# Kernel optimization log

Measured on AMD Instinct MI355X. Metric: run time of the kernel, lower is better.

## Reference

```python
import jax, jax.numpy as jnp
import numpy as np

N, E, IN, H, OUT = 50000, 800000, 256, 128, 64


def setup_inputs() -> dict:
    key = jax.random.key(0)
    ks = jax.random.split(key, 4)
    x = jax.random.normal(ks[0], (N, IN), dtype=jnp.float32)
    edge_index = jax.random.randint(ks[1], (2, E), 0, N, dtype=jnp.int64)
    W1 = jax.random.normal(ks[2], (IN, H), dtype=jnp.float32) / np.float32(np.sqrt(IN))
    b1 = jnp.zeros((H,), jnp.float32)
    W2 = jax.random.normal(ks[3], (H, OUT), dtype=jnp.float32) / np.float32(np.sqrt(H))
    b2 = jnp.zeros((OUT,), jnp.float32)
    return {"x": x, "edge_index": edge_index, "W1": W1, "b1": b1, "W2": W2, "b2": b2}


def _gcn_conv(x, W, b, src, dst, norm, n):
    # PyG GCNConv: linear transform, then symmetric-normalized aggregation, then bias
    h = x @ W                                        # [n, d_out]
    agg = jax.ops.segment_sum(h[src] * norm[:, None], dst, num_segments=n)
    return agg + b


def reference(x, edge_index, W1, b1, W2, b2):
    n = x.shape[0]
    loop = jnp.arange(n, dtype=edge_index.dtype)
    # add self-loops (GCNConv default add_self_loops=True)
    src = jnp.concatenate([edge_index[0], loop])
    dst = jnp.concatenate([edge_index[1], loop])
    # symmetric normalization deg^{-1/2} A_hat deg^{-1/2}
    deg = jax.ops.segment_sum(jnp.ones(src.shape, jnp.float32), dst, num_segments=n)
    dinv = jnp.where(deg > 0, jax.lax.rsqrt(deg), 0.0)
    norm = dinv[src] * dinv[dst]                     # [E + n]
    h = jax.nn.relu(_gcn_conv(x, W1, b1, src, dst, norm, n))
    return _gcn_conv(h, W2, b2, src, dst, norm, n)
```

## Files before the change

### kernel.cpp

```cpp
#include <hip/hip_runtime.h>


#define DI 256
#define DH 128
#define DO 64
#define NBC 98
#define EPB 8192
#define P4CAP 12288

typedef unsigned short ushort;
typedef unsigned int uint;
using bf16x8 = __attribute__((ext_vector_type(8))) short;
using f32x4  = __attribute__((ext_vector_type(4))) float;

__device__ __forceinline__ ushort f2b(float f) {
    union { float f; uint u; } v; v.f = f;
    uint r = (v.u + 0x7fffu + ((v.u >> 16) & 1u)) >> 16;
    return (ushort)r;
}
__device__ __forceinline__ float blo(uint v) { return __uint_as_float(v << 16); }
__device__ __forceinline__ float bhi(uint v) { return __uint_as_float(v & 0xffff0000u); }

__global__ __launch_bounds__(256) void hist_k(const int* __restrict__ dst,
                                              int* __restrict__ hist, int E,
                                              const float* __restrict__ W1,
                                              ushort* __restrict__ W1t,
                                              const float* __restrict__ W2,
                                              ushort* __restrict__ W2t) {
    __shared__ int lh[NBC];
    const int blk = blockIdx.x;
    for (int i = threadIdx.x; i < NBC; i += 256) lh[i] = 0;
    __syncthreads();
    const int gid = blk * 256 + threadIdx.x;
#pragma unroll
    for (int r = 0; r < 2; ++r) {
        int idx = gid + r * 25088;
        if (idx < DI * DH) {
            int m = idx / DI, k = idx % DI;
            W1t[idx] = f2b(W1[(long)k * DH + m]);
        }
    }
    if (gid < DH * DO) {
        int m = gid / DH, k = gid % DH;
        W2t[gid] = f2b(W2[(long)k * DO + m]);
    }
    const int base = blk * EPB, end = min(base + EPB, E);
    for (int e = base + threadIdx.x; e < end; e += 256)
        atomicAdd(&lh[dst[e] >> 9], 1);
    __syncthreads();
    for (int i = threadIdx.x; i < NBC; i += 256) hist[blk * NBC + i] = lh[i];
}

__global__ void scan_mat(int* __restrict__ hist, int* __restrict__ boff,
                         int* __restrict__ off, int nbp, int n, int E) {
    __shared__ int mat[NBC * NBC];
    __shared__ int tot[NBC], bo[NBC];
    const int tid = threadIdx.x;
    const int tote = nbp * NBC;
    for (int i = tid; i < tote; i += 256) mat[i] = hist[i];
    __syncthreads();
    if (tid < NBC) {
        int run = 0;
        for (int b = 0; b < nbp; ++b) {
            int v = mat[b * NBC + tid];
            mat[b * NBC + tid] = run;
            run += v;
        }
        tot[tid] = run;
    }
    __syncthreads();
    if (tid == 0) {
        int r = 0;
        for (int c = 0; c < NBC; ++c) { bo[c] = r; r += tot[c]; }
        boff[NBC] = r;
        off[n] = E;
    }
    __syncthreads();
    if (tid < NBC) boff[tid] = bo[tid];
    for (int i = tid; i < tote; i += 256) hist[i] = mat[i] + bo[i % NBC];
}

__global__ __launch_bounds__(256) void part_k(const int* __restrict__ src,
                                              const int* __restrict__ dst,
                                              const int* __restrict__ hist,
                                              uint* __restrict__ pairs, int E) {
    __shared__ int cur[NBC];
    const int blk = blockIdx.x;
    for (int i = threadIdx.x; i < NBC; i += 256) cur[i] = hist[blk * NBC + i];
    __syncthreads();
    const int base = blk * EPB, end = min(base + EPB, E);
    for (int e = base + threadIdx.x; e < end; e += 256) {
        int d = dst[e], s = src[e];
        int slot = atomicAdd(&cur[d >> 9], 1);
        pairs[slot] = ((uint)s << 9) | (uint)(d & 511);
    }
}

__global__ __launch_bounds__(256) void bucket_k(const uint* __restrict__ pairs,
                                                const int* __restrict__ boff,
                                                int* __restrict__ off,
                                                float* __restrict__ dinv,
                                                int* __restrict__ csr, int n) {
    __shared__ int lh[512], lcur[512], tsum[256];
    __shared__ int sorted[P4CAP];
    const int tid = threadIdx.x;
    const int cb = blockIdx.x;
    const int b0 = boff[cb], b1 = boff[cb + 1];
    const int cnt = b1 - b0;
    lh[tid] = 0; lh[tid + 256] = 0;
    __syncthreads();
    for (int i = tid; i < cnt; i += 256) atomicAdd(&lh[pairs[b0 + i] & 511], 1);
    __syncthreads();
    const int s0 = lh[2 * tid], s1 = lh[2 * tid + 1];
    const int s = s0 + s1;
    tsum[tid] = s;
    __syncthreads();
    for (int o = 1; o < 256; o <<= 1) {
        int t = (tid >= o) ? tsum[tid - o] : 0;
        __syncthreads();
        tsum[tid] += t;
        __syncthreads();
    }
    const int ex = tsum[tid] - s;
    lcur[2 * tid] = ex; lcur[2 * tid + 1] = ex + s0;
    {
        int node = cb * 512 + 2 * tid;
        if (node < n)     { off[node]     = b0 + ex;      dinv[node]     = rsqrtf((float)s0 + 1.f); }
        if (node + 1 < n) { off[node + 1] = b0 + ex + s0; dinv[node + 1] = rsqrtf((float)s1 + 1.f); }
    }
    __syncthreads();
    for (int i = tid; i < cnt; i += 256) {
        uint v = pairs[b0 + i];
        int slot = atomicAdd(&lcur[v & 511], 1);
        if (slot < P4CAP) sorted[slot] = (int)(v >> 9);
    }
    __syncthreads();
    const int cs = min(cnt, P4CAP);
    for (int i = tid; i < cs; i += 256) csr[b0 + i] = sorted[i];
}

template<int K, int M, bool INF32>
__global__ __launch_bounds__(256) void mfma_gemm(const void* __restrict__ Xv,
                                                 const ushort* __restrict__ Wt,
                                                 const float* __restrict__ dinv,
                                                 ushort* __restrict__ Y, int n) {
    constexpr int ROWB = K * 2;
    constexpr int CT = M / 64;
    __shared__ ushort Xs[64 * K];
    const int t = threadIdx.x;
    const int r0 = blockIdx.x * 64;

    {
        const int row = t >> 2, q = t & 3;
        const int gr = r0 + row;
        if (INF32) {
            const float* Xr = (const float*)Xv + (long)gr * K;
#pragma unroll
            for (int j = 0; j < K / 32; ++j) {
                float4 a = make_float4(0.f, 0.f, 0.f, 0.f), b = a;
                if (gr < n) {
                    a = *(const float4*)&Xr[q * 8 + j * 32];
                    b = *(const float4*)&Xr[q * 8 + j * 32 + 4];
                }
                ushort u[8] = {f2b(a.x), f2b(a.y), f2b(a.z), f2b(a.w),
                               f2b(b.x), f2b(b.y), f2b(b.z), f2b(b.w)};
                int byte = row * ROWB + q * 16 + j * 64;
                byte ^= (row & 7) << 4;
                *(uint4*)((char*)Xs + byte) = *(const uint4*)u;
            }
        } else {
            const ushort* Xr = (const ushort*)Xv + (long)gr * K;
#pragma unroll
            for (int j = 0; j < K / 32; ++j) {
                uint4 v = make_uint4(0u, 0u, 0u, 0u);
                if (gr < n) v = *(const uint4*)&Xr[q * 8 + j * 32];
                int byte = row * ROWB + q * 16 + j * 64;
                byte ^= (row & 7) << 4;
                *(uint4*)((char*)Xs + byte) = v;
            }
        }
    }
    __syncthreads();

    const int w  = t >> 6;
    const int l  = t & 63;
    const int lr = l & 15;
    const int lg = l >> 4;
    f32x4 acc[4][CT] = {};

#pragma unroll
    for (int ks = 0; ks < K / 32; ++ks) {
        bf16x8 bfr[CT];
#pragma unroll
        for (int ct = 0; ct < CT; ++ct) {
            int col = w * (M / 4) + ct * 16 + lr;
            bfr[ct] = *(const bf16x8*)&Wt[(long)col * K + ks * 32 + lg * 8];
        }
        bf16x8 afr[4];
#pragma unroll
        for (int rt = 0; rt < 4; ++rt) {
            int row = rt * 16 + lr;
            int byte = row * ROWB + ks * 64 + lg * 16;
            byte ^= (row & 7) << 4;
            afr[rt] = *(const bf16x8*)((const char*)Xs + byte);
        }
#pragma unroll
        for (int rt = 0; rt < 4; ++rt)
#pragma unroll
            for (int ct = 0; ct < CT; ++ct)
                acc[rt][ct] = __builtin_amdgcn_mfma_f32_16x16x32_bf16(
                    afr[rt], bfr[ct], acc[rt][ct], 0, 0, 0);
    }

#pragma unroll
    for (int rt = 0; rt < 4; ++rt)
#pragma unroll
        for (int i = 0; i < 4; ++i) {
            int gr2 = r0 + rt * 16 + lg * 4 + i;
            if (gr2 < n) {
                float dv = dinv[gr2];
#pragma unroll
                for (int ct = 0; ct < CT; ++ct) {
                    int col = w * (M / 4) + ct * 16 + lr;
                    Y[(long)gr2 * M + col] = f2b(dv * acc[rt][ct][i]);
                }
            }
        }
}

__global__ __launch_bounds__(256) void gather_half(const int* __restrict__ off,
                                                   const int* __restrict__ csr,
                                                   const ushort* __restrict__ Hs,
                                                   const float* __restrict__ dinv,
                                                   const float* __restrict__ b1,
                                                   ushort* __restrict__ h, int n) {
    const int wv = threadIdx.x >> 6, ln = threadIdx.x & 63;
    const int grp = ln >> 3, j = ln & 7;
    const int half = blockIdx.x & 1;
    const int i = (blockIdx.x >> 1) * 4 + wv;
    if (i >= n) return;
    const uint4* H4 = (const uint4*)Hs;
    const int cb = half * 8 + j;
    float a0[8] = {}, a1[8] = {};
    const int k0 = off[i], ke = off[i + 1];
    int k = k0 + grp;
    for (; k + 8 < ke; k += 16) {
        uint4 va = H4[(long)csr[k] * 16 + cb];
        uint4 vb = H4[(long)csr[k + 8] * 16 + cb];
        a0[0] += blo(va.x); a0[1] += bhi(va.x);
        a0[2] += blo(va.y); a0[3] += bhi(va.y);
        a0[4] += blo(va.z); a0[5] += bhi(va.z);
        a0[6] += blo(va.w); a0[7] += bhi(va.w);
        a1[0] += blo(vb.x); a1[1] += bhi(vb.x);
        a1[2] += blo(vb.y); a1[3] += bhi(vb.y);
        a1[4] += blo(vb.z); a1[5] += bhi(vb.z);
        a1[6] += blo(vb.w); a1[7] += bhi(vb.w);
    }
    if (k < ke) {
        uint4 va = H4[(long)csr[k] * 16 + cb];
        a0[0] += blo(va.x); a0[1] += bhi(va.x);
        a0[2] += blo(va.y); a0[3] += bhi(va.y);
        a0[4] += blo(va.z); a0[5] += bhi(va.z);
        a0[6] += blo(va.w); a0[7] += bhi(va.w);
    }
    if (grp == 0) {
        uint4 va = H4[(long)i * 16 + cb];
        a1[0] += blo(va.x); a1[1] += bhi(va.x);
        a1[2] += blo(va.y); a1[3] += bhi(va.y);
        a1[4] += blo(va.z); a1[5] += bhi(va.z);
        a1[6] += blo(va.w); a1[7] += bhi(va.w);
    }
    float acc[8];
#pragma unroll
    for (int m = 0; m < 8; ++m) {
        acc[m] = a0[m] + a1[m];
        acc[m] += __shfl_xor(acc[m], 8, 64);
        acc[m] += __shfl_xor(acc[m], 16, 64);
        acc[m] += __shfl_xor(acc[m], 32, 64);
    }
    if (grp == 0) {
        float di = dinv[i];
        float4 bb0 = ((const float4*)b1)[cb * 2];
        float4 bb1 = ((const float4*)b1)[cb * 2 + 1];
        ushort u[8];
        u[0] = f2b(fmaxf(di * acc[0] + bb0.x, 0.f));
        u[1] = f2b(fmaxf(di * acc[1] + bb0.y, 0.f));
        u[2] = f2b(fmaxf(di * acc[2] + bb0.z, 0.f));
        u[3] = f2b(fmaxf(di * acc[3] + bb0.w, 0.f));
        u[4] = f2b(fmaxf(di * acc[4] + bb1.x, 0.f));
        u[5] = f2b(fmaxf(di * acc[5] + bb1.y, 0.f));
        u[6] = f2b(fmaxf(di * acc[6] + bb1.z, 0.f));
        u[7] = f2b(fmaxf(di * acc[7] + bb1.w, 0.f));
        *(uint4*)&h[(long)i * DH + cb * 8] = *(const uint4*)u;
    }
}

__global__ __launch_bounds__(256) void gather_out(const int* __restrict__ off,
                                                  const int* __restrict__ csr,
                                                  const ushort* __restrict__ Hs,
                                                  const float* __restrict__ dinv,
                                                  const float* __restrict__ b,
                                                  float* __restrict__ Y, int n) {
    const int wv = threadIdx.x >> 6, ln = threadIdx.x & 63;
    const int grp = ln >> 3, j = ln & 7;
    const int i = blockIdx.x * 4 + wv;
    if (i >= n) return;
    const uint4* H4 = (const uint4*)Hs;
    float a0[8] = {}, a1[8] = {}, a2[8] = {}, a3[8] = {};
    const int k0 = off[i], ke = off[i + 1];
    int k = k0 + grp;
    for (; k + 24 < ke; k += 32) {
        uint4 va = H4[(long)csr[k]      * 8 + j];
        uint4 vb = H4[(long)csr[k + 8]  * 8 + j];
        uint4 vc = H4[(long)csr[k + 16] * 8 + j];
        uint4 vd = H4[(long)csr[k + 24] * 8 + j];
        a0[0] += blo(va.x); a0[1] += bhi(va.x); a0[2] += blo(va.y); a0[3] += bhi(va.y);
        a0[4] += blo(va.z); a0[5] += bhi(va.z); a0[6] += blo(va.w); a0[7] += bhi(va.w);
        a1[0] += blo(vb.x); a1[1] += bhi(vb.x); a1[2] += blo(vb.y); a1[3] += bhi(vb.y);
        a1[4] += blo(vb.z); a1[5] += bhi(vb.z); a1[6] += blo(vb.w); a1[7] += bhi(vb.w);
        a2[0] += blo(vc.x); a2[1] += bhi(vc.x); a2[2] += blo(vc.y); a2[3] += bhi(vc.y);
        a2[4] += blo(vc.z); a2[5] += bhi(vc.z); a2[6] += blo(vc.w); a2[7] += bhi(vc.w);
        a3[0] += blo(vd.x); a3[1] += bhi(vd.x); a3[2] += blo(vd.y); a3[3] += bhi(vd.y);
        a3[4] += blo(vd.z); a3[5] += bhi(vd.z); a3[6] += blo(vd.w); a3[7] += bhi(vd.w);
    }
    for (; k < ke; k += 8) {
        uint4 va = H4[(long)csr[k] * 8 + j];
        a0[0] += blo(va.x); a0[1] += bhi(va.x); a0[2] += blo(va.y); a0[3] += bhi(va.y);
        a0[4] += blo(va.z); a0[5] += bhi(va.z); a0[6] += blo(va.w); a0[7] += bhi(va.w);
    }
    if (grp == 0) {
        uint4 va = H4[(long)i * 8 + j];
        a1[0] += blo(va.x); a1[1] += bhi(va.x); a1[2] += blo(va.y); a1[3] += bhi(va.y);
        a1[4] += blo(va.z); a1[5] += bhi(va.z); a1[6] += blo(va.w); a1[7] += bhi(va.w);
    }
    float acc[8];
#pragma unroll
    for (int m = 0; m < 8; ++m) {
        acc[m] = (a0[m] + a1[m]) + (a2[m] + a3[m]);
        acc[m] += __shfl_xor(acc[m], 8, 64);
        acc[m] += __shfl_xor(acc[m], 16, 64);
        acc[m] += __shfl_xor(acc[m], 32, 64);
    }
    if (grp == 0) {
        float di = dinv[i];
        float4 b0 = ((const float4*)b)[j * 2];
        float4 b1 = ((const float4*)b)[j * 2 + 1];
        float4 o0, o1;
        o0.x = di * acc[0] + b0.x; o0.y = di * acc[1] + b0.y;
        o0.z = di * acc[2] + b0.z; o0.w = di * acc[3] + b0.w;
        o1.x = di * acc[4] + b1.x; o1.y = di * acc[5] + b1.y;
        o1.z = di * acc[6] + b1.z; o1.w = di * acc[7] + b1.w;
        *(float4*)&Y[(long)i * DO + j * 8]     = o0;
        *(float4*)&Y[(long)i * DO + j * 8 + 4] = o1;
    }
}

extern "C" void kernel_launch(void* const* d_in, const int* in_sizes, int n_in,
                              void* d_out, int out_size, void* d_ws, size_t ws_size,
                              hipStream_t stream) {
    const float* x  = (const float*)d_in[0];
    const int*   ei = (const int*)d_in[1];
    const float* W1 = (const float*)d_in[2];
    const float* b1 = (const float*)d_in[3];
    const float* W2 = (const float*)d_in[4];
    const float* b2 = (const float*)d_in[5];
    float* out = (float*)d_out;

    const int n = in_sizes[0] / DI;
    const int E = in_sizes[1] / 2;
    const int* src = ei;
    const int* dst = ei + E;
    const int np  = ((n + 255) / 256) * 256;
    const int nbp = (E + EPB - 1) / EPB;
    const int nbc = (n + 511) >> 9;

    int*    hist  = (int*)d_ws;
    int*    boff  = hist + NBC * NBC;
    int*    off   = boff + 128;
    float*  dinv  = (float*)(off + np + 256);
    int*    csr   = (int*)(dinv + np);
    uint*   pairs = (uint*)(csr + E);
    ushort* w1t   = (ushort*)(pairs + E);
    ushort* w2t   = w1t + DH * DI;
    ushort* h0s   = w2t + DO * DH;
    ushort* h     = h0s + (size_t)n * DH;
    ushort* h1s   = h + (size_t)n * DH;

    hist_k<<<nbp, 256, 0, stream>>>(dst, hist, E, W1, w1t, W2, w2t);
    scan_mat<<<1, 256, 0, stream>>>(hist, boff, off, nbp, n, E);
    part_k<<<nbp, 256, 0, stream>>>(src, dst, hist, pairs, E);
    bucket_k<<<nbc, 256, 0, stream>>>(pairs, boff, off, dinv, csr, n);

    const int gblk = (n + 63) / 64;
    mfma_gemm<DI, DH, true><<<gblk, 256, 0, stream>>>(x, w1t, dinv, h0s, n);
    gather_half<<<2 * ((n + 3) / 4), 256, 0, stream>>>(off, csr, h0s, dinv, b1, h, n);
    mfma_gemm<DH, DO, false><<<gblk, 256, 0, stream>>>(h, w2t, dinv, h1s, n);
    gather_out<<<(n + 3) / 4, 256, 0, stream>>>(off, csr, h1s, dinv, b2, out, n);
}
```

Measured before the change: 252.2 us.

## Fuse layer-1 aggregation with the second GEMM via shared-memory MFMA tile

Replaces the separate gather_half kernel and the second mfma_gemm with one kernel. It aggregates 16 nodes' neighbour rows into a swizzled shared-memory tile with bias and ReLU applied, then multiplies that tile by W2 with bf16 MFMA. This removes one launch and the write and re-read of the intermediate hidden matrix h. In exchange, each wave now walks four nodes in sequence with 16 lanes per row instead of splitting feature halves across blocks, and the grid has fewer blocks, so gather parallelism and latency hiding may drop.

```diff
diff --git a/kernel.cpp b/kernel.cpp
--- a/kernel.cpp
+++ b/kernel.cpp
@@ -20,6 +20,12 @@
 }
 __device__ __forceinline__ float blo(uint v) { return __uint_as_float(v << 16); }
 __device__ __forceinline__ float bhi(uint v) { return __uint_as_float(v & 0xffff0000u); }
+__device__ __forceinline__ void acc8(float* a, uint4 v) {
+    a[0] += blo(v.x); a[1] += bhi(v.x);
+    a[2] += blo(v.y); a[3] += bhi(v.y);
+    a[4] += blo(v.z); a[5] += bhi(v.z);
+    a[6] += blo(v.w); a[7] += bhi(v.w);
+}
 
 __global__ __launch_bounds__(256) void hist_k(const int* __restrict__ dst,
                                               int* __restrict__ hist, int E,
@@ -228,70 +234,85 @@
         }
 }
 
-__global__ __launch_bounds__(256) void gather_half(const int* __restrict__ off,
-                                                   const int* __restrict__ csr,
-                                                   const ushort* __restrict__ Hs,
-                                                   const float* __restrict__ dinv,
-                                                   const float* __restrict__ b1,
-                                                   ushort* __restrict__ h, int n) {
-    const int wv = threadIdx.x >> 6, ln = threadIdx.x & 63;
-    const int grp = ln >> 3, j = ln & 7;
-    const int half = blockIdx.x & 1;
-    const int i = (blockIdx.x >> 1) * 4 + wv;
-    if (i >= n) return;
+__global__ __launch_bounds__(256) void gather_gemm2(const int* __restrict__ off,
+                                                    const int* __restrict__ csr,
+                                                    const ushort* __restrict__ Hs,
+                                                    const float* __restrict__ dinv,
+                                                    const float* __restrict__ b1,
+                                                    const ushort* __restrict__ W2t,
+                                                    ushort* __restrict__ h1s, int n) {
+    __shared__ ushort Xs[16 * DH];
+    const int tid = threadIdx.x;
+    const int wv = tid >> 6, ln = tid & 63;
+    const int grp = ln >> 4, j = ln & 15;
+    const int base = blockIdx.x * 16;
     const uint4* H4 = (const uint4*)Hs;
-    const int cb = half * 8 + j;
-    float a0[8] = {}, a1[8] = {};
-    const int k0 = off[i], ke = off[i + 1];
-    int k = k0 + grp;
-    for (; k + 8 < ke; k += 16) {
-        uint4 va = H4[(long)csr[k] * 16 + cb];
-        uint4 vb = H4[(long)csr[k + 8] * 16 + cb];
-        a0[0] += blo(va.x); a0[1] += bhi(va.x);
-        a0[2] += blo(va.y); a0[3] += bhi(va.y);
-        a0[4] += blo(va.z); a0[5] += bhi(va.z);
-        a0[6] += blo(va.w); a0[7] += bhi(va.w);
-        a1[0] += blo(vb.x); a1[1] += bhi(vb.x);
-        a1[2] += blo(vb.y); a1[3] += bhi(vb.y);
-        a1[4] += blo(vb.z); a1[5] += bhi(vb.z);
-        a1[6] += blo(vb.w); a1[7] += bhi(vb.w);
-    }
-    if (k < ke) {
-        uint4 va = H4[(long)csr[k] * 16 + cb];
-        a0[0] += blo(va.x); a0[1] += bhi(va.x);
-        a0[2] += blo(va.y); a0[3] += bhi(va.y);
-        a0[4] += blo(va.z); a0[5] += bhi(va.z);
-        a0[6] += blo(va.w); a0[7] += bhi(va.w);
-    }
-    if (grp == 0) {
-        uint4 va = H4[(long)i * 16 + cb];
-        a1[0] += blo(va.x); a1[1] += bhi(va.x);
-        a1[2] += blo(va.y); a1[3] += bhi(va.y);
-        a1[4] += blo(va.z); a1[5] += bhi(va.z);
-        a1[6] += blo(va.w); a1[7] += bhi(va.w);
-    }
-    float acc[8];
-#pragma unroll
-    for (int m = 0; m < 8; ++m) {
-        acc[m] = a0[m] + a1[m];
-        acc[m] += __shfl_xor(acc[m], 8, 64);
-        acc[m] += __shfl_xor(acc[m], 16, 64);
-        acc[m] += __shfl_xor(acc[m], 32, 64);
-    }
-    if (grp == 0) {
-        float di = dinv[i];
-        float4 bb0 = ((const float4*)b1)[cb * 2];
-        float4 bb1 = ((const float4*)b1)[cb * 2 + 1];
-        ushort u[8];
-        u[0] = f2b(fmaxf(di * acc[0] + bb0.x, 0.f));
-        u[1] = f2b(fmaxf(di * acc[1] + bb0.y, 0.f));
-        u[2] = f2b(fmaxf(di * acc[2] + bb0.z, 0.f));
-        u[3] = f2b(fmaxf(di * acc[3] + bb0.w, 0.f));
-        u[4] = f2b(fmaxf(di * acc[4] + bb1.x, 0.f));
-        u[5] = f2b(fmaxf(di * acc[5] + bb1.y, 0.f));
-        u[6] = f2b(fmaxf(di * acc[6] + bb1.z, 0.f));
-        u[7] = f2b(fmaxf(di * acc[7] + bb1.w, 0.f));
-        *(uint4*)&h[(long)i * DH + cb * 8] = *(const uint4*)u;
+
+#pragma unroll
+    for (int q = 0; q < 4; ++q) {
+        const int row = wv * 4 + q;
+        const int node = base + row;
+        float a0[8] = {}, a1[8] = {}, a2[8] = {}, a3[8] = {};
+        if (node < n) {
+            const int k0 = off[node], ke = off[node + 1];
+            int k = k0 + grp;
+            for (; k + 12 < ke; k += 16) {
+                uint4 va = H4[(long)csr[k]      * 16 + j];
+                uint4 vb = H4[(long)csr[k + 4]  * 16 + j];
+                uint4 vc = H4[(long)csr[k + 8]  * 16 + j];
+                uint4 vd = H4[(long)csr[k + 12] * 16 + j];
+                acc8(a0, va); acc8(a1, vb); acc8(a2, vc); acc8(a3, vd);
+            }
+            for (; k < ke; k += 4) {
+                uint4 va = H4[(long)csr[k] * 16 + j];
+                acc8(a0, va);
+            }
+            if (grp == 0) {
+                uint4 va = H4[(long)node * 16 + j];
+                acc8(a1, va);
+            }
+        }
+        float r[8];
+#pragma unroll
+        for (int m = 0; m < 8; ++m) {
+            r[m] = (a0[m] + a1[m]) + (a2[m] + a3[m]);
+            r[m] += __shfl_xor(r[m], 16, 64);
+            r[m] += __shfl_xor(r[m], 32, 64);
+        }
+        if (grp == 0 && node < n) {
+            float di = dinv[node];
+            float4 bb0 = ((const float4*)b1)[j * 2];
+            float4 bb1 = ((const float4*)b1)[j * 2 + 1];
+            ushort u[8];
+            u[0] = f2b(fmaxf(di * r[0] + bb0.x, 0.f));
+            u[1] = f2b(fmaxf(di * r[1] + bb0.y, 0.f));
+            u[2] = f2b(fmaxf(di * r[2] + bb0.z, 0.f));
+            u[3] = f2b(fmaxf(di * r[3] + bb0.w, 0.f));
+            u[4] = f2b(fmaxf(di * r[4] + bb1.x, 0.f));
+            u[5] = f2b(fmaxf(di * r[5] + bb1.y, 0.f));
+            u[6] = f2b(fmaxf(di * r[6] + bb1.z, 0.f));
+            u[7] = f2b(fmaxf(di * r[7] + bb1.w, 0.f));
+            int byte = row * 256 + j * 16;
+            byte ^= (row & 7) << 4;
+            *(uint4*)((char*)Xs + byte) = *(const uint4*)u;
+        }
+    }
+    __syncthreads();
+
+    const int lr = ln & 15, lg = ln >> 4;
+    f32x4 acc = {};
+#pragma unroll
+    for (int ks = 0; ks < 4; ++ks) {
+        bf16x8 bfr = *(const bf16x8*)&W2t[(wv * 16 + lr) * DH + ks * 32 + lg * 8];
+        int byte = lr * 256 + ks * 64 + lg * 16;
+        byte ^= (lr & 7) << 4;
+        bf16x8 afr = *(const bf16x8*)((const char*)Xs + byte);
+        acc = __builtin_amdgcn_mfma_f32_16x16x32_bf16(afr, bfr, acc, 0, 0, 0);
+    }
+#pragma unroll
+    for (int i = 0; i < 4; ++i) {
+        int r2 = base + lg * 4 + i;
+        if (r2 < n) h1s[(long)r2 * DO + wv * 16 + lr] = f2b(dinv[r2] * acc[i]);
     }
 }
 
@@ -314,24 +335,15 @@
         uint4 vb = H4[(long)csr[k + 8]  * 8 + j];
         uint4 vc = H4[(long)csr[k + 16] * 8 + j];
         uint4 vd = H4[(long)csr[k + 24] * 8 + j];
-        a0[0] += blo(va.x); a0[1] += bhi(va.x); a0[2] += blo(va.y); a0[3] += bhi(va.y);
-        a0[4] += blo(va.z); a0[5] += bhi(va.z); a0[6] += blo(va.w); a0[7] += bhi(va.w);
-        a1[0] += blo(vb.x); a1[1] += bhi(vb.x); a1[2] += blo(vb.y); a1[3] += bhi(vb.y);
-        a1[4] += blo(vb.z); a1[5] += bhi(vb.z); a1[6] += blo(vb.w); a1[7] += bhi(vb.w);
-        a2[0] += blo(vc.x); a2[1] += bhi(vc.x); a2[2] += blo(vc.y); a2[3] += bhi(vc.y);
-        a2[4] += blo(vc.z); a2[5] += bhi(vc.z); a2[6] += blo(vc.w); a2[7] += bhi(vc.w);
-        a3[0] += blo(vd.x); a3[1] += bhi(vd.x); a3[2] += blo(vd.y); a3[3] += bhi(vd.y);
-        a3[4] += blo(vd.z); a3[5] += bhi(vd.z); a3[6] += blo(vd.w); a3[7] += bhi(vd.w);
+        acc8(a0, va); acc8(a1, vb); acc8(a2, vc); acc8(a3, vd);
     }
     for (; k < ke; k += 8) {
         uint4 va = H4[(long)csr[k] * 8 + j];
-        a0[0] += blo(va.x); a0[1] += bhi(va.x); a0[2] += blo(va.y); a0[3] += bhi(va.y);
-        a0[4] += blo(va.z); a0[5] += bhi(va.z); a0[6] += blo(va.w); a0[7] += bhi(va.w);
+        acc8(a0, va);
     }
     if (grp == 0) {
         uint4 va = H4[(long)i * 8 + j];
-        a1[0] += blo(va.x); a1[1] += bhi(va.x); a1[2] += blo(va.y); a1[3] += bhi(va.y);
-        a1[4] += blo(va.z); a1[5] += bhi(va.z); a1[6] += blo(va.w); a1[7] += bhi(va.w);
+        acc8(a1, va);
     }
     float acc[8];
 #pragma unroll
@@ -383,8 +395,7 @@
     ushort* w1t   = (ushort*)(pairs + E);
     ushort* w2t   = w1t + DH * DI;
     ushort* h0s   = w2t + DO * DH;
-    ushort* h     = h0s + (size_t)n * DH;
-    ushort* h1s   = h + (size_t)n * DH;
+    ushort* h1s   = h0s + (size_t)n * DH;
 
     hist_k<<<nbp, 256, 0, stream>>>(dst, hist, E, W1, w1t, W2, w2t);
     scan_mat<<<1, 256, 0, stream>>>(hist, boff, off, nbp, n, E);
@@ -393,7 +404,6 @@
 
     const int gblk = (n + 63) / 64;
     mfma_gemm<DI, DH, true><<<gblk, 256, 0, stream>>>(x, w1t, dinv, h0s, n);
-    gather_half<<<2 * ((n + 3) / 4), 256, 0, stream>>>(off, csr, h0s, dinv, b1, h, n);
-    mfma_gemm<DH, DO, false><<<gblk, 256, 0, stream>>>(h, w2t, dinv, h1s, n);
+    gather_gemm2<<<(n + 15) / 16, 256, 0, stream>>>(off, csr, h0s, dinv, b1, w2t, h1s, n);
     gather_out<<<(n + 3) / 4, 256, 0, stream>>>(off, csr, h1s, dinv, b2, out, n);
 }
```

After: 245.8 us. 2.5% less time.

## Fold scan into partition kernels, scatter CSR directly, remap gather thread layouts

Applied to the files above, without the earlier changes.

The single-block scan_mat kernel is removed; part_k and bucket_k each recompute their bucket offsets from the histogram matrix with a redundant in-block prefix scan, saving one launch and a serial single-block stage. bucket_k drops its shared-memory staging buffer and scatters source indices directly into the global CSR array, which removes the capacity cap and frees LDS but makes the writes scattered. The layer-1 gather now covers all 128 features in one wave per node with 4 edge groups instead of two half-blocks, and the output gather packs two nodes per wave with 4 edge groups each. Together these rebalance edge-level parallelism against memory-level parallelism and cut redundant edge-index reads.

```diff
diff --git a/kernel.cpp b/kernel.cpp
--- a/kernel.cpp
+++ b/kernel.cpp
@@ -6,7 +6,6 @@
 #define DO 64
 #define NBC 98
 #define EPB 8192
-#define P4CAP 12288
 
 typedef unsigned short ushort;
 typedef unsigned int uint;
@@ -20,6 +19,12 @@
 }
 __device__ __forceinline__ float blo(uint v) { return __uint_as_float(v << 16); }
 __device__ __forceinline__ float bhi(uint v) { return __uint_as_float(v & 0xffff0000u); }
+__device__ __forceinline__ void acc8(float* a, uint4 v) {
+    a[0] += blo(v.x); a[1] += bhi(v.x);
+    a[2] += blo(v.y); a[3] += bhi(v.y);
+    a[4] += blo(v.z); a[5] += bhi(v.z);
+    a[6] += blo(v.w); a[7] += bhi(v.w);
+}
 
 __global__ __launch_bounds__(256) void hist_k(const int* __restrict__ dst,
                                               int* __restrict__ hist, int E,
@@ -51,45 +56,35 @@
     for (int i = threadIdx.x; i < NBC; i += 256) hist[blk * NBC + i] = lh[i];
 }
 
-__global__ void scan_mat(int* __restrict__ hist, int* __restrict__ boff,
-                         int* __restrict__ off, int nbp, int n, int E) {
-    __shared__ int mat[NBC * NBC];
-    __shared__ int tot[NBC], bo[NBC];
-    const int tid = threadIdx.x;
-    const int tote = nbp * NBC;
-    for (int i = tid; i < tote; i += 256) mat[i] = hist[i];
-    __syncthreads();
-    if (tid < NBC) {
-        int run = 0;
-        for (int b = 0; b < nbp; ++b) {
-            int v = mat[b * NBC + tid];
-            mat[b * NBC + tid] = run;
-            run += v;
-        }
-        tot[tid] = run;
-    }
-    __syncthreads();
-    if (tid == 0) {
-        int r = 0;
-        for (int c = 0; c < NBC; ++c) { bo[c] = r; r += tot[c]; }
-        boff[NBC] = r;
-        off[n] = E;
-    }
-    __syncthreads();
-    if (tid < NBC) boff[tid] = bo[tid];
-    for (int i = tid; i < tote; i += 256) hist[i] = mat[i] + bo[i % NBC];
-}
-
 __global__ __launch_bounds__(256) void part_k(const int* __restrict__ src,
                                               const int* __restrict__ dst,
                                               const int* __restrict__ hist,
-                                              uint* __restrict__ pairs, int E) {
+                                              uint* __restrict__ pairs,
+                                              int nbp, int E) {
     __shared__ int cur[NBC];
+    __shared__ int tsum[256];
     const int blk = blockIdx.x;
-    for (int i = threadIdx.x; i < NBC; i += 256) cur[i] = hist[blk * NBC + i];
+    const int t = threadIdx.x;
+    int tot = 0, p = 0;
+    if (t < NBC) {
+        for (int b = 0; b < nbp; ++b) {
+            int v = hist[b * NBC + t];
+            if (b < blk) p += v;
+            tot += v;
+        }
+    }
+    tsum[t] = tot;
+    __syncthreads();
+    for (int o = 1; o < 256; o <<= 1) {
+        int v = (t >= o) ? tsum[t - o] : 0;
+        __syncthreads();
+        tsum[t] += v;
+        __syncthreads();
+    }
+    if (t < NBC) cur[t] = (tsum[t] - tot) + p;
     __syncthreads();
     const int base = blk * EPB, end = min(base + EPB, E);
-    for (int e = base + threadIdx.x; e < end; e += 256) {
+    for (int e = base + t; e < end; e += 256) {
         int d = dst[e], s = src[e];
         int slot = atomicAdd(&cur[d >> 9], 1);
         pairs[slot] = ((uint)s << 9) | (uint)(d & 511);
@@ -97,18 +92,32 @@
 }
 
 __global__ __launch_bounds__(256) void bucket_k(const uint* __restrict__ pairs,
-                                                const int* __restrict__ boff,
+                                                const int* __restrict__ hist,
                                                 int* __restrict__ off,
                                                 float* __restrict__ dinv,
-                                                int* __restrict__ csr, int n) {
+                                                int* __restrict__ csr,
+                                                int nbp, int n, int E) {
     __shared__ int lh[512], lcur[512], tsum[256];
-    __shared__ int sorted[P4CAP];
     const int tid = threadIdx.x;
     const int cb = blockIdx.x;
-    const int b0 = boff[cb], b1 = boff[cb + 1];
-    const int cnt = b1 - b0;
+    int tot = 0;
+    if (tid < NBC) {
+        for (int b = 0; b < nbp; ++b) tot += hist[b * NBC + tid];
+    }
+    tsum[tid] = tot;
+    __syncthreads();
+    for (int o = 1; o < 256; o <<= 1) {
+        int v = (tid >= o) ? tsum[tid - o] : 0;
+        __syncthreads();
+        tsum[tid] += v;
+        __syncthreads();
+    }
+    __shared__ int b0s, cnts;
+    if (tid == cb) { b0s = tsum[tid] - tot; cnts = tot; }
+    if (cb == 0 && tid == 0) off[n] = E;
     lh[tid] = 0; lh[tid + 256] = 0;
     __syncthreads();
+    const int b0 = b0s, cnt = cnts;
     for (int i = tid; i < cnt; i += 256) atomicAdd(&lh[pairs[b0 + i] & 511], 1);
     __syncthreads();
     const int s0 = lh[2 * tid], s1 = lh[2 * tid + 1];
@@ -116,13 +125,13 @@
     tsum[tid] = s;
     __syncthreads();
     for (int o = 1; o < 256; o <<= 1) {
-        int t = (tid >= o) ? tsum[tid - o] : 0;
-        __syncthreads();
-        tsum[tid] += t;
+        int v = (tid >= o) ? tsum[tid - o] : 0;
+        __syncthreads();
+        tsum[tid] += v;
         __syncthreads();
     }
     const int ex = tsum[tid] - s;
-    lcur[2 * tid] = ex; lcur[2 * tid + 1] = ex + s0;
+    lcur[2 * tid] = b0 + ex; lcur[2 * tid + 1] = b0 + ex + s0;
     {
         int node = cb * 512 + 2 * tid;
         if (node < n)     { off[node]     = b0 + ex;      dinv[node]     = rsqrtf((float)s0 + 1.f); }
@@ -132,11 +141,8 @@
     for (int i = tid; i < cnt; i += 256) {
         uint v = pairs[b0 + i];
         int slot = atomicAdd(&lcur[v & 511], 1);
-        if (slot < P4CAP) sorted[slot] = (int)(v >> 9);
-    }
-    __syncthreads();
-    const int cs = min(cnt, P4CAP);
-    for (int i = tid; i < cs; i += 256) csr[b0 + i] = sorted[i];
+        csr[slot] = (int)(v >> 9);
+    }
 }
 
 template<int K, int M, bool INF32>
@@ -228,60 +234,40 @@
         }
 }
 
-__global__ __launch_bounds__(256) void gather_half(const int* __restrict__ off,
-                                                   const int* __restrict__ csr,
-                                                   const ushort* __restrict__ Hs,
-                                                   const float* __restrict__ dinv,
-                                                   const float* __restrict__ b1,
-                                                   ushort* __restrict__ h, int n) {
+__global__ __launch_bounds__(256) void gather_h(const int* __restrict__ off,
+                                                const int* __restrict__ csr,
+                                                const ushort* __restrict__ Hs,
+                                                const float* __restrict__ dinv,
+                                                const float* __restrict__ b1,
+                                                ushort* __restrict__ h, int n) {
     const int wv = threadIdx.x >> 6, ln = threadIdx.x & 63;
-    const int grp = ln >> 3, j = ln & 7;
-    const int half = blockIdx.x & 1;
-    const int i = (blockIdx.x >> 1) * 4 + wv;
+    const int grp = ln >> 4, j = ln & 15;
+    const int i = blockIdx.x * 4 + wv;
     if (i >= n) return;
     const uint4* H4 = (const uint4*)Hs;
-    const int cb = half * 8 + j;
-    float a0[8] = {}, a1[8] = {};
+    float a0[8] = {}, a1[8] = {}, a2[8] = {}, a3[8] = {};
     const int k0 = off[i], ke = off[i + 1];
     int k = k0 + grp;
-    for (; k + 8 < ke; k += 16) {
-        uint4 va = H4[(long)csr[k] * 16 + cb];
-        uint4 vb = H4[(long)csr[k + 8] * 16 + cb];
-        a0[0] += blo(va.x); a0[1] += bhi(va.x);
-        a0[2] += blo(va.y); a0[3] += bhi(va.y);
-        a0[4] += blo(va.z); a0[5] += bhi(va.z);
-        a0[6] += blo(va.w); a0[7] += bhi(va.w);
-        a1[0] += blo(vb.x); a1[1] += bhi(vb.x);
-        a1[2] += blo(vb.y); a1[3] += bhi(vb.y);
-        a1[4] += blo(vb.z); a1[5] += bhi(vb.z);
-        a1[6] += blo(vb.w); a1[7] += bhi(vb.w);
-    }
-    if (k < ke) {
-        uint4 va = H4[(long)csr[k] * 16 + cb];
-        a0[0] += blo(va.x); a0[1] += bhi(va.x);
-        a0[2] += blo(va.y); a0[3] += bhi(va.y);
-        a0[4] += blo(va.z); a0[5] += bhi(va.z);
-        a0[6] += blo(va.w); a0[7] += bhi(va.w);
-    }
-    if (grp == 0) {
-        uint4 va = H4[(long)i * 16 + cb];
-        a1[0] += blo(va.x); a1[1] += bhi(va.x);
-        a1[2] += blo(va.y); a1[3] += bhi(va.y);
-        a1[4] += blo(va.z); a1[5] += bhi(va.z);
-        a1[6] += blo(va.w); a1[7] += bhi(va.w);
-    }
+    for (; k + 12 < ke; k += 16) {
+        uint4 va = H4[(long)csr[k]      * 16 + j];
+        uint4 vb = H4[(long)csr[k + 4]  * 16 + j];
+        uint4 vc = H4[(long)csr[k + 8]  * 16 + j];
+        uint4 vd = H4[(long)csr[k + 12] * 16 + j];
+        acc8(a0, va); acc8(a1, vb); acc8(a2, vc); acc8(a3, vd);
+    }
+    for (; k < ke; k += 4) acc8(a0, H4[(long)csr[k] * 16 + j]);
+    if (grp == 0) acc8(a1, H4[(long)i * 16 + j]);
     float acc[8];
 #pragma unroll
     for (int m = 0; m < 8; ++m) {
-        acc[m] = a0[m] + a1[m];
-        acc[m] += __shfl_xor(acc[m], 8, 64);
+        acc[m] = (a0[m] + a1[m]) + (a2[m] + a3[m]);
         acc[m] += __shfl_xor(acc[m], 16, 64);
         acc[m] += __shfl_xor(acc[m], 32, 64);
     }
     if (grp == 0) {
         float di = dinv[i];
-        float4 bb0 = ((const float4*)b1)[cb * 2];
-        float4 bb1 = ((const float4*)b1)[cb * 2 + 1];
+        float4 bb0 = ((const float4*)b1)[j * 2];
+        float4 bb1 = ((const float4*)b1)[j * 2 + 1];
         ushort u[8];
         u[0] = f2b(fmaxf(di * acc[0] + bb0.x, 0.f));
         u[1] = f2b(fmaxf(di * acc[1] + bb0.y, 0.f));
@@ -291,7 +277,7 @@
         u[5] = f2b(fmaxf(di * acc[5] + bb1.y, 0.f));
         u[6] = f2b(fmaxf(di * acc[6] + bb1.z, 0.f));
         u[7] = f2b(fmaxf(di * acc[7] + bb1.w, 0.f));
-        *(uint4*)&h[(long)i * DH + cb * 8] = *(const uint4*)u;
+        *(uint4*)&h[(long)i * DH + j * 8] = *(const uint4*)u;
     }
 }
 
@@ -302,44 +288,27 @@
                                                   const float* __restrict__ b,
                                                   float* __restrict__ Y, int n) {
     const int wv = threadIdx.x >> 6, ln = threadIdx.x & 63;
-    const int grp = ln >> 3, j = ln & 7;
-    const int i = blockIdx.x * 4 + wv;
+    const int half = ln >> 5, l5 = ln & 31;
+    const int grp = l5 >> 3, j = l5 & 7;
+    const int i = blockIdx.x * 8 + wv * 2 + half;
     if (i >= n) return;
     const uint4* H4 = (const uint4*)Hs;
-    float a0[8] = {}, a1[8] = {}, a2[8] = {}, a3[8] = {};
+    float a0[8] = {}, a1[8] = {};
     const int k0 = off[i], ke = off[i + 1];
     int k = k0 + grp;
-    for (; k + 24 < ke; k += 32) {
-        uint4 va = H4[(long)csr[k]      * 8 + j];
-        uint4 vb = H4[(long)csr[k + 8]  * 8 + j];
-        uint4 vc = H4[(long)csr[k + 16] * 8 + j];
-        uint4 vd = H4[(long)csr[k + 24] * 8 + j];
-        a0[0] += blo(va.x); a0[1] += bhi(va.x); a0[2] += blo(va.y); a0[3] += bhi(va.y);
-        a0[4] += blo(va.z); a0[5] += bhi(va.z); a0[6] += blo(va.w); a0[7] += bhi(va.w);
-        a1[0] += blo(vb.x); a1[1] += bhi(vb.x); a1[2] += blo(vb.y); a1[3] += bhi(vb.y);
-        a1[4] += blo(vb.z); a1[5] += bhi(vb.z); a1[6] += blo(vb.w); a1[7] += bhi(vb.w);
-        a2[0] += blo(vc.x); a2[1] += bhi(vc.x); a2[2] += blo(vc.y); a2[3] += bhi(vc.y);
-        a2[4] += blo(vc.z); a2[5] += bhi(vc.z); a2[6] += blo(vc.w); a2[7] += bhi(vc.w);
-        a3[0] += blo(vd.x); a3[1] += bhi(vd.x); a3[2] += blo(vd.y); a3[3] += bhi(vd.y);
-        a3[4] += blo(vd.z); a3[5] += bhi(vd.z); a3[6] += blo(vd.w); a3[7] += bhi(vd.w);
-    }
-    for (; k < ke; k += 8) {
-        uint4 va = H4[(long)csr[k] * 8 + j];
-        a0[0] += blo(va.x); a0[1] += bhi(va.x); a0[2] += blo(va.y); a0[3] += bhi(va.y);
-        a0[4] += blo(va.z); a0[5] += bhi(va.z); a0[6] += blo(va.w); a0[7] += bhi(va.w);
-    }
-    if (grp == 0) {
-        uint4 va = H4[(long)i * 8 + j];
-        a1[0] += blo(va.x); a1[1] += bhi(va.x); a1[2] += blo(va.y); a1[3] += bhi(va.y);
-        a1[4] += blo(va.z); a1[5] += bhi(va.z); a1[6] += blo(va.w); a1[7] += bhi(va.w);
-    }
+    for (; k + 4 < ke; k += 8) {
+        uint4 va = H4[(long)csr[k]     * 8 + j];
+        uint4 vb = H4[(long)csr[k + 4] * 8 + j];
+        acc8(a0, va); acc8(a1, vb);
+    }
+    if (k < ke) acc8(a0, H4[(long)csr[k] * 8 + j]);
+    if (grp == 0) acc8(a1, H4[(long)i * 8 + j]);
     float acc[8];
 #pragma unroll
     for (int m = 0; m < 8; ++m) {
-        acc[m] = (a0[m] + a1[m]) + (a2[m] + a3[m]);
+        acc[m] = a0[m] + a1[m];
         acc[m] += __shfl_xor(acc[m], 8, 64);
         acc[m] += __shfl_xor(acc[m], 16, 64);
-        acc[m] += __shfl_xor(acc[m], 32, 64);
     }
     if (grp == 0) {
         float di = dinv[i];
@@ -375,8 +344,7 @@
     const int nbc = (n + 511) >> 9;
 
     int*    hist  = (int*)d_ws;
-    int*    boff  = hist + NBC * NBC;
-    int*    off   = boff + 128;
+    int*    off   = hist + NBC * NBC;
     float*  dinv  = (float*)(off + np + 256);
     int*    csr   = (int*)(dinv + np);
     uint*   pairs = (uint*)(csr + E);
@@ -387,13 +355,12 @@
     ushort* h1s   = h + (size_t)n * DH;
 
     hist_k<<<nbp, 256, 0, stream>>>(dst, hist, E, W1, w1t, W2, w2t);
-    scan_mat<<<1, 256, 0, stream>>>(hist, boff, off, nbp, n, E);
-    part_k<<<nbp, 256, 0, stream>>>(src, dst, hist, pairs, E);
-    bucket_k<<<nbc, 256, 0, stream>>>(pairs, boff, off, dinv, csr, n);
+    part_k<<<nbp, 256, 0, stream>>>(src, dst, hist, pairs, nbp, E);
+    bucket_k<<<nbc, 256, 0, stream>>>(pairs, hist, off, dinv, csr, nbp, n, E);
 
     const int gblk = (n + 63) / 64;
     mfma_gemm<DI, DH, true><<<gblk, 256, 0, stream>>>(x, w1t, dinv, h0s, n);
-    gather_half<<<2 * ((n + 3) / 4), 256, 0, stream>>>(off, csr, h0s, dinv, b1, h, n);
+    gather_h<<<(n + 3) / 4, 256, 0, stream>>>(off, csr, h0s, dinv, b1, h, n);
     mfma_gemm<DH, DO, false><<<gblk, 256, 0, stream>>>(h, w2t, dinv, h1s, n);
-    gather_out<<<(n + 3) / 4, 256, 0, stream>>>(off, csr, h1s, dinv, b2, out, n);
-}
+    gather_out<<<(n + 7) / 8, 256, 0, stream>>>(off, csr, h1s, dinv, b2, out, n);
+}
```

After: 248.6 us. Within noise of the previous version (-1.4%).
